# Kernel tuning notes

Measured on AMD Instinct MI355X. Metric: run time of the kernel, lower is better.

The kernel has to match this reference:

```python
import jax, jax.numpy as jnp
import numpy as np

# snntorch atan surrogate (alpha=2): forward heaviside, backward 1/(1+(pi*x)^2)
@jax.custom_vjp
def atan_spike(x):
    return (x > 0).astype(x.dtype)

def _atan_fwd(x):
    return atan_spike(x), x

def _atan_bwd(x, g):
    return (g / (1.0 + (jnp.pi * x) ** 2),)

atan_spike.defvjp(_atan_fwd, _atan_bwd)

B, S, D, H = 8, 2048, 1024, 1024

def setup_inputs() -> dict:
    key = jax.random.key(0)
    ks = jax.random.split(key, 6)
    s = 0.02
    return {
        "x": jax.random.normal(ks[0], (B, S, D), jnp.float32),
        "w_ih": jax.random.normal(ks[1], (4 * H, D), jnp.float32) * s,  # LSTMCell input weights (gate order i,f,g,o)
        "w_hh": jax.random.normal(ks[2], (4 * H, H), jnp.float32) * s,
        "b_ih": jnp.zeros((4 * H,), jnp.float32),
        "b_hh": jnp.zeros((4 * H,), jnp.float32),
        "w_fc": jax.random.normal(ks[3], (H, H), jnp.float32) * s,
        "b_fc": jnp.zeros((H,), jnp.float32),
        "threshold": jnp.float32(1.0),   # learn_threshold=True, init 1.0
        "dyt_alpha": jnp.float32(0.5),   # DynamicTanh alpha
        "dyt_w": jnp.ones((H,), jnp.float32),
        "dyt_b": jnp.zeros((H,), jnp.float32),
    }

def reference(x, w_ih, w_hh, b_ih, b_hh, w_fc, b_fc, threshold, dyt_alpha, dyt_w, dyt_b):
    # Precompute input-to-gate projection for all timesteps: (B,S,4H)
    x_ih = jnp.einsum("bsd,gd->bsg", x, w_ih) + b_ih

    def step(carry, inp):
        syn, mem = carry          # cell state, hidden/membrane state (B,H)
        x_t, g_ih = inp
        # subtract-reset based on PREVIOUS mem, detached (snntorch mem_reset)
        reset = jax.lax.stop_gradient((mem - threshold > 0).astype(mem.dtype))
        gates = g_ih + mem @ w_hh.T + b_hh
        i, f, g, o = jnp.split(gates, 4, axis=-1)
        c = jax.nn.sigmoid(f) * syn + jax.nn.sigmoid(i) * jnp.tanh(g)
        h = jax.nn.sigmoid(o) * jnp.tanh(c)
        mem_new = h - reset * threshold
        spk = atan_spike(mem_new - threshold)
        out = spk @ w_fc.T + b_fc + x_t                 # fc + residual
        out = dyt_w * jnp.tanh(dyt_alpha * out) + dyt_b  # Dyt normalizer
        return (c, mem_new), out

    syn0 = jnp.zeros((x.shape[0], w_fc.shape[0]), x.dtype)
    mem0 = jnp.zeros((x.shape[0], w_fc.shape[0]), x.dtype)
    (syn, mem), out = jax.lax.scan(
        step, (syn0, mem0),
        (jnp.swapaxes(x, 0, 1), jnp.swapaxes(x_ih, 0, 1)))
    return jnp.swapaxes(out, 0, 1), syn, mem
```

## Files before the change

kernel.cpp:

```cpp
#include <hip/hip_runtime.h>

#define NB 8
#define NS 2048
#define ND 1024
#define NH 1024
#define NWG 256
#define TPB 512
#define HPW 4
#define PSTRIDE 20

#define SCOPE_AGENT __HIP_MEMORY_SCOPE_AGENT

__device__ __forceinline__ float sigmf(float v)     { return 1.f / (1.f + __expf(-v)); }
__device__ __forceinline__ float tanh_fast(float v) { return 1.f - 2.f / (1.f + __expf(2.f * v)); }

#define DOT4(acc, W, V)                 \
    acc = fmaf((W).x, (V).x, acc);      \
    acc = fmaf((W).y, (V).y, acc);      \
    acc = fmaf((W).z, (V).z, acc);      \
    acc = fmaf((W).w, (V).w, acc);

__global__ __launch_bounds__(TPB, 2)
void scan_kernel(const float* __restrict__ x,
                 const float* __restrict__ w_ih,
                 const float* __restrict__ w_hh,
                 const float* __restrict__ b_ih,
                 const float* __restrict__ b_hh,
                 const float* __restrict__ thrp,
                 unsigned long long* __restrict__ membuf,
                 unsigned long long* __restrict__ bitmap,
                 float* __restrict__ out_syn,
                 float* __restrict__ out_mem)
{
    __shared__ float x_s2[2][NB * NH];
    __shared__ float m_s[NB * NH];
    __shared__ float sgm[16 * NB * PSTRIDE];
    __shared__ float sgx[2][16 * NB * PSTRIDE];
    __shared__ float bias_s[16];

    const int tid   = threadIdx.x;
    const int wg    = blockIdx.x;
    const int wave  = tid >> 6;
    const int lane  = tid & 63;
    const int g     = wave & 3;
    const bool ismem = (wave < 4);
    const float thr = *thrp;

    float4 wt[4][4];
    {
        const float* WM = ismem ? w_hh : w_ih;
        #pragma unroll
        for (int rl = 0; rl < 4; ++rl) {
            const int R = g * NH + wg * HPW + rl;
            #pragma unroll
            for (int j = 0; j < 4; ++j)
                wt[rl][j] = *(const float4*)(WM + (size_t)R * ND + j * 256 + lane * 4);
        }
    }
    if (tid < 16) {
        const int R = (tid >> 2) * NH + wg * HPW + (tid & 3);
        bias_s[tid] = b_ih[R] + b_hh[R];
    }
    float c_reg = 0.f;

    auto xdots = [&](int slot) {
        const float4* xs4 = (const float4*)x_s2[slot];
        #pragma unroll
        for (int b = 0; b < NB; ++b) {
            float4 xv[4];
            #pragma unroll
            for (int j = 0; j < 4; ++j) xv[j] = xs4[b * 256 + j * 64 + lane];
            float a0 = 0.f, a1 = 0.f, a2 = 0.f, a3 = 0.f;
            #pragma unroll
            for (int j = 0; j < 4; ++j) {
                DOT4(a0, wt[0][j], xv[j]);
                DOT4(a1, wt[1][j], xv[j]);
                DOT4(a2, wt[2][j], xv[j]);
                DOT4(a3, wt[3][j], xv[j]);
            }
            a0 += __shfl_xor(a0, 1); a0 += __shfl_xor(a0, 2);
            a1 += __shfl_xor(a1, 1); a1 += __shfl_xor(a1, 2);
            a2 += __shfl_xor(a2, 1); a2 += __shfl_xor(a2, 2);
            a3 += __shfl_xor(a3, 1); a3 += __shfl_xor(a3, 2);
            if ((lane & 3) == 0) {
                const int p = lane >> 2;
                float* dst = &sgx[slot][0];
                dst[((g * 4 + 0) * NB + b) * PSTRIDE + p] = a0;
                dst[((g * 4 + 1) * NB + b) * PSTRIDE + p] = a1;
                dst[((g * 4 + 2) * NB + b) * PSTRIDE + p] = a2;
                dst[((g * 4 + 3) * NB + b) * PSTRIDE + p] = a3;
            }
        }
    };

    auto prefetch = [&](int slot, int t1) {
        #pragma unroll
        for (int i = 0; i < 4; ++i) {
            const int q = i * 8 + wave;
            const int chunk = q * 64 + lane;
            const int b = chunk >> 8, d = (chunk & 255) * 4;
            __builtin_amdgcn_global_load_lds(
                (const __attribute__((address_space(1))) unsigned int*)(x + ((size_t)b * NS + t1) * ND + d),
                (__attribute__((address_space(3))) unsigned int*)&x_s2[slot][q * 256],
                16, 0, 0);
        }
    };

    prefetch(0, 0);
    __syncthreads();
    if (!ismem) xdots(0);

    for (int t = 0; t < NS; ++t) {
        const unsigned long long* mc = membuf + (size_t)(t & 1) * (NB * NH);
        unsigned long long*       mn64 = membuf + (size_t)((t + 1) & 1) * (NB * NH);

        if (t < NS - 1) prefetch((t + 1) & 1, t + 1);

        {
            const unsigned want = (unsigned)t;
            unsigned long long warr[16];
            #pragma unroll
            for (int k = 0; k < 16; ++k)
                warr[k] = __hip_atomic_load(mc + tid + k * TPB,
                                            __ATOMIC_RELAXED, SCOPE_AGENT);
            unsigned pend = 0;
            #pragma unroll
            for (int k = 0; k < 16; ++k) {
                if ((unsigned)(warr[k] >> 32) == want)
                    m_s[tid + k * TPB] = __uint_as_float((unsigned)warr[k]);
                else
                    pend |= (1u << k);
            }
            while (pend) {
                unsigned long long w2[16];
                unsigned np = 0;
                #pragma unroll
                for (int k = 0; k < 16; ++k)
                    if (pend & (1u << k))
                        w2[k] = __hip_atomic_load(mc + tid + k * TPB,
                                                  __ATOMIC_RELAXED, SCOPE_AGENT);
                #pragma unroll
                for (int k = 0; k < 16; ++k)
                    if (pend & (1u << k)) {
                        if ((unsigned)(w2[k] >> 32) == want)
                            m_s[tid + k * TPB] = __uint_as_float((unsigned)w2[k]);
                        else
                            np |= (1u << k);
                    }
                pend = np;
            }
        }
        __syncthreads();

        if (ismem) {
            const float4* ms4 = (const float4*)m_s;
            #pragma unroll
            for (int b = 0; b < NB; ++b) {
                float4 mv[4];
                #pragma unroll
                for (int j = 0; j < 4; ++j) mv[j] = ms4[b * 256 + j * 64 + lane];
                float a0 = 0.f, a1 = 0.f, a2 = 0.f, a3 = 0.f;
                #pragma unroll
                for (int j = 0; j < 4; ++j) {
                    DOT4(a0, wt[0][j], mv[j]);
                    DOT4(a1, wt[1][j], mv[j]);
                    DOT4(a2, wt[2][j], mv[j]);
                    DOT4(a3, wt[3][j], mv[j]);
                }
                a0 += __shfl_xor(a0, 1); a0 += __shfl_xor(a0, 2);
                a1 += __shfl_xor(a1, 1); a1 += __shfl_xor(a1, 2);
                a2 += __shfl_xor(a2, 1); a2 += __shfl_xor(a2, 2);
                a3 += __shfl_xor(a3, 1); a3 += __shfl_xor(a3, 2);
                if ((lane & 3) == 0) {
                    const int p = lane >> 2;
                    sgm[((g * 4 + 0) * NB + b) * PSTRIDE + p] = a0;
                    sgm[((g * 4 + 1) * NB + b) * PSTRIDE + p] = a1;
                    sgm[((g * 4 + 2) * NB + b) * PSTRIDE + p] = a2;
                    sgm[((g * 4 + 3) * NB + b) * PSTRIDE + p] = a3;
                }
            }
        } else if (t < NS - 1) {
            xdots((t + 1) & 1);
        }
        __syncthreads();

        if (tid < 32) {
            const int hl = tid >> 3, b = tid & 7;
            const int h  = wg * HPW + hl;
            float gv[4];
            #pragma unroll
            for (int gg = 0; gg < 4; ++gg) {
                const int r = gg * 4 + hl;
                const float4* pm = (const float4*)&sgm[(r * NB + b) * PSTRIDE];
                const float4* px = (const float4*)&sgx[t & 1][(r * NB + b) * PSTRIDE];
                float s = bias_s[r];
                #pragma unroll
                for (int q = 0; q < 4; ++q) {
                    float4 vm = pm[q], vx = px[q];
                    s += vm.x + vm.y + vm.z + vm.w + vx.x + vx.y + vx.z + vx.w;
                }
                gv[gg] = s;
            }
            const float cn = sigmf(gv[1]) * c_reg + sigmf(gv[0]) * tanh_fast(gv[2]);
            const float hv = sigmf(gv[3]) * tanh_fast(cn);
            const float mprev = m_s[b * NH + h];
            const float reset = (mprev - thr > 0.f) ? 1.f : 0.f;
            const float mn = hv - reset * thr;
            c_reg = cn;
            const unsigned long long pk =
                ((unsigned long long)(unsigned)(t + 1) << 32) | __float_as_uint(mn);
            __hip_atomic_store(mn64 + b * NH + h, pk, __ATOMIC_RELAXED, SCOPE_AGENT);
            if (mn - thr > 0.f)
                atomicOr(bitmap + (size_t)(b * NS + t) * (NH / 64) + (h >> 6),
                         1ull << (h & 63));
            if (t == NS - 1) {
                out_syn[b * NH + h] = cn;
                out_mem[b * NH + h] = mn;
            }
        }
        __syncthreads();
    }
}

__global__ __launch_bounds__(256)
void out_kernel(const float* __restrict__ x,
                const float* __restrict__ b_fc,
                const float* __restrict__ w_fc,
                const float* __restrict__ alphap,
                const float* __restrict__ dytw,
                const float* __restrict__ dytb,
                const unsigned long long* __restrict__ bitmap,
                float* __restrict__ out)
{
    __shared__ unsigned long long wds[16];
    __shared__ int flag;
    const int row = blockIdx.x;
    const int tid = threadIdx.x;
    if (tid < 16) wds[tid] = bitmap[(size_t)row * 16 + tid];
    __syncthreads();
    if (tid == 0) {
        unsigned long long o = 0ull;
        #pragma unroll
        for (int i = 0; i < 16; ++i) o |= wds[i];
        flag = (o != 0ull);
    }
    __syncthreads();

    const float alpha = *alphap;
    const float* xr = x + (size_t)row * NH;
    float* orow = out + (size_t)row * NH;
    const int j0 = tid * 4;

    float4 xv = *(const float4*)(xr + j0);
    float4 bf = *(const float4*)(b_fc + j0);
    float4 dw = *(const float4*)(dytw + j0);
    float4 db = *(const float4*)(dytb + j0);
    float p[4]   = {xv.x, xv.y, xv.z, xv.w};
    float bfa[4] = {bf.x, bf.y, bf.z, bf.w};
    float dwa[4] = {dw.x, dw.y, dw.z, dw.w};
    float dba[4] = {db.x, db.y, db.z, db.w};

    #pragma unroll
    for (int u = 0; u < 4; ++u) {
        float v = p[u] + bfa[u];
        if (flag) {
            const int j = j0 + u;
            for (int wi = 0; wi < 16; ++wi) {
                unsigned long long m = wds[wi];
                while (m) {
                    int bit = __ffsll(m) - 1;
                    m &= m - 1;
                    v += w_fc[(size_t)j * NH + wi * 64 + bit];
                }
            }
        }
        p[u] = dwa[u] * tanh_fast(alpha * v) + dba[u];
    }
    *(float4*)(orow + j0) = make_float4(p[0], p[1], p[2], p[3]);
}

extern "C" void kernel_launch(void* const* d_in, const int* in_sizes, int n_in,
                              void* d_out, int out_size, void* d_ws, size_t ws_size,
                              hipStream_t stream) {
    const float* x     = (const float*)d_in[0];
    const float* w_ih  = (const float*)d_in[1];
    const float* w_hh  = (const float*)d_in[2];
    const float* b_ih  = (const float*)d_in[3];
    const float* b_hh  = (const float*)d_in[4];
    const float* w_fc  = (const float*)d_in[5];
    const float* b_fc  = (const float*)d_in[6];
    const float* thr   = (const float*)d_in[7];
    const float* alpha = (const float*)d_in[8];
    const float* dytw  = (const float*)d_in[9];
    const float* dytb  = (const float*)d_in[10];

    float* out  = (float*)d_out;
    float* syn  = out + (size_t)NB * NS * NH;
    float* memf = syn + (size_t)NB * NH;

    char* ws = (char*)d_ws;
    unsigned long long* membuf = (unsigned long long*)ws;
    unsigned long long* bitmap = (unsigned long long*)(ws + 131072);

    size_t zbytes = 131072 + (size_t)NB * NS * (NH / 64) * 8;
    (void)hipMemsetAsync(d_ws, 0, zbytes, stream);

    hipLaunchKernelGGL(scan_kernel, dim3(NWG), dim3(TPB), 0, stream,
                       x, w_ih, w_hh, b_ih, b_hh, thr, membuf, bitmap, syn, memf);
    hipLaunchKernelGGL(out_kernel, dim3(NB * NS), dim3(256), 0, stream,
                       x, b_fc, w_fc, alpha, dytw, dytb, bitmap, out);
}
```

Baseline: 12.96 ms.

## Split batch across workgroup groups and pack recurrent state as tagged bf16

The 256 workgroups are split into two batch groups. Each workgroup now handles 4 batches and 8 hidden units with 1024 threads, instead of 8 batches and 4 hidden units. The exchanged membrane state shrinks from 64-bit (tag + fp32) to 32-bit (16-bit step tag + bf16 value). It is polled with one dwordx4 load per thread plus a sleep-backoff retry loop. This is meant to cut the per-step global read and sync traffic in the serial recurrence. The cost is reduced precision on the recurrent mem input to the w_hh matmul, which could flip spike decisions near threshold.

```diff
diff --git a/kernel.cpp b/kernel.cpp
--- a/kernel.cpp
+++ b/kernel.cpp
@@ -5,8 +5,9 @@
 #define ND 1024
 #define NH 1024
 #define NWG 256
-#define TPB 512
-#define HPW 4
+#define TPB 1024
+#define NBG 4
+#define HPW 8
 #define PSTRIDE 20
 
 #define SCOPE_AGENT __HIP_MEMORY_SCOPE_AGENT
@@ -20,30 +21,43 @@
     acc = fmaf((W).z, (V).z, acc);      \
     acc = fmaf((W).w, (V).w, acc);
 
-__global__ __launch_bounds__(TPB, 2)
+__device__ __forceinline__ float bf16_unpack(unsigned w) {
+    return __uint_as_float((w & 0xFFFFu) << 16);
+}
+__device__ __forceinline__ unsigned bf16_rne(float f) {
+    unsigned b = __float_as_uint(f);
+    return (b + 0x7FFFu + ((b >> 16) & 1u)) >> 16;
+}
+
+__global__ __launch_bounds__(TPB, 4)
 void scan_kernel(const float* __restrict__ x,
                  const float* __restrict__ w_ih,
                  const float* __restrict__ w_hh,
                  const float* __restrict__ b_ih,
                  const float* __restrict__ b_hh,
                  const float* __restrict__ thrp,
-                 unsigned long long* __restrict__ membuf,
+                 unsigned* __restrict__ membuf,
                  unsigned long long* __restrict__ bitmap,
                  float* __restrict__ out_syn,
                  float* __restrict__ out_mem)
 {
-    __shared__ float x_s2[2][NB * NH];
-    __shared__ float m_s[NB * NH];
-    __shared__ float sgm[16 * NB * PSTRIDE];
-    __shared__ float sgx[2][16 * NB * PSTRIDE];
-    __shared__ float bias_s[16];
+    __shared__ float x_s2[2][NBG * NH];
+    __shared__ float m_s[NBG * NH];
+    __shared__ float sgm[32 * NBG * PSTRIDE];
+    __shared__ float sgx[2][32 * NBG * PSTRIDE];
+    __shared__ float bias_s[32];
 
     const int tid   = threadIdx.x;
     const int wg    = blockIdx.x;
+    const int grpb  = wg >> 7;
+    const int wgl   = wg & 127;
+    const int hb    = wgl * HPW;
     const int wave  = tid >> 6;
     const int lane  = tid & 63;
-    const int g     = wave & 3;
-    const bool ismem = (wave < 4);
+    const bool ismem = (wave < 8);
+    const int wx    = wave & 7;
+    const int g     = wx & 3;
+    const int hh0   = (wx >> 2) * 4;
     const float thr = *thrp;
 
     float4 wt[4][4];
@@ -51,14 +65,14 @@
         const float* WM = ismem ? w_hh : w_ih;
         #pragma unroll
         for (int rl = 0; rl < 4; ++rl) {
-            const int R = g * NH + wg * HPW + rl;
+            const int R = g * NH + hb + hh0 + rl;
             #pragma unroll
             for (int j = 0; j < 4; ++j)
                 wt[rl][j] = *(const float4*)(WM + (size_t)R * ND + j * 256 + lane * 4);
         }
     }
-    if (tid < 16) {
-        const int R = (tid >> 2) * NH + wg * HPW + (tid & 3);
+    if (tid < 32) {
+        const int R = (tid >> 3) * NH + hb + (tid & 7);
         bias_s[tid] = b_ih[R] + b_hh[R];
     }
     float c_reg = 0.f;
@@ -66,10 +80,10 @@
     auto xdots = [&](int slot) {
         const float4* xs4 = (const float4*)x_s2[slot];
         #pragma unroll
-        for (int b = 0; b < NB; ++b) {
+        for (int bl = 0; bl < NBG; ++bl) {
             float4 xv[4];
             #pragma unroll
-            for (int j = 0; j < 4; ++j) xv[j] = xs4[b * 256 + j * 64 + lane];
+            for (int j = 0; j < 4; ++j) xv[j] = xs4[bl * 256 + j * 64 + lane];
             float a0 = 0.f, a1 = 0.f, a2 = 0.f, a3 = 0.f;
             #pragma unroll
             for (int j = 0; j < 4; ++j) {
@@ -85,25 +99,22 @@
             if ((lane & 3) == 0) {
                 const int p = lane >> 2;
                 float* dst = &sgx[slot][0];
-                dst[((g * 4 + 0) * NB + b) * PSTRIDE + p] = a0;
-                dst[((g * 4 + 1) * NB + b) * PSTRIDE + p] = a1;
-                dst[((g * 4 + 2) * NB + b) * PSTRIDE + p] = a2;
-                dst[((g * 4 + 3) * NB + b) * PSTRIDE + p] = a3;
+                const int r0 = g * 8 + hh0;
+                dst[((r0 + 0) * NBG + bl) * PSTRIDE + p] = a0;
+                dst[((r0 + 1) * NBG + bl) * PSTRIDE + p] = a1;
+                dst[((r0 + 2) * NBG + bl) * PSTRIDE + p] = a2;
+                dst[((r0 + 3) * NBG + bl) * PSTRIDE + p] = a3;
             }
         }
     };
 
     auto prefetch = [&](int slot, int t1) {
-        #pragma unroll
-        for (int i = 0; i < 4; ++i) {
-            const int q = i * 8 + wave;
-            const int chunk = q * 64 + lane;
-            const int b = chunk >> 8, d = (chunk & 255) * 4;
-            __builtin_amdgcn_global_load_lds(
-                (const __attribute__((address_space(1))) unsigned int*)(x + ((size_t)b * NS + t1) * ND + d),
-                (__attribute__((address_space(3))) unsigned int*)&x_s2[slot][q * 256],
-                16, 0, 0);
-        }
+        const int bl = tid >> 8, d = (tid & 255) * 4;
+        __builtin_amdgcn_global_load_lds(
+            (const __attribute__((address_space(1))) unsigned int*)
+                (x + ((size_t)(grpb * NBG + bl) * NS + t1) * ND + d),
+            (__attribute__((address_space(3))) unsigned int*)&x_s2[slot][tid * 4],
+            16, 0, 0);
     };
 
     prefetch(0, 0);
@@ -111,43 +122,28 @@
     if (!ismem) xdots(0);
 
     for (int t = 0; t < NS; ++t) {
-        const unsigned long long* mc = membuf + (size_t)(t & 1) * (NB * NH);
-        unsigned long long*       mn64 = membuf + (size_t)((t + 1) & 1) * (NB * NH);
-
-        if (t < NS - 1) prefetch((t + 1) & 1, t + 1);
+        const int cs = t & 1, ns_ = (t + 1) & 1;
+        const unsigned* mc = membuf + (size_t)(cs * 8 + grpb * NBG) * NH;
+        unsigned*       mp = membuf + (size_t)(ns_ * 8 + grpb * NBG) * NH;
+
+        if (t < NS - 1) prefetch(ns_, t + 1);
 
         {
             const unsigned want = (unsigned)t;
-            unsigned long long warr[16];
-            #pragma unroll
-            for (int k = 0; k < 16; ++k)
-                warr[k] = __hip_atomic_load(mc + tid + k * TPB,
-                                            __ATOMIC_RELAXED, SCOPE_AGENT);
-            unsigned pend = 0;
-            #pragma unroll
-            for (int k = 0; k < 16; ++k) {
-                if ((unsigned)(warr[k] >> 32) == want)
-                    m_s[tid + k * TPB] = __uint_as_float((unsigned)warr[k]);
-                else
-                    pend |= (1u << k);
-            }
-            while (pend) {
-                unsigned long long w2[16];
-                unsigned np = 0;
-                #pragma unroll
-                for (int k = 0; k < 16; ++k)
-                    if (pend & (1u << k))
-                        w2[k] = __hip_atomic_load(mc + tid + k * TPB,
-                                                  __ATOMIC_RELAXED, SCOPE_AGENT);
-                #pragma unroll
-                for (int k = 0; k < 16; ++k)
-                    if (pend & (1u << k)) {
-                        if ((unsigned)(w2[k] >> 32) == want)
-                            m_s[tid + k * TPB] = __uint_as_float((unsigned)w2[k]);
-                        else
-                            np |= (1u << k);
-                    }
-                pend = np;
+            uint4 v;
+            asm volatile(
+                "global_load_dwordx4 %0, %1, off sc0 sc1\n\t"
+                "s_waitcnt vmcnt(0)"
+                : "=&v"(v) : "v"(mc + tid * 4) : "memory");
+            unsigned w0 = v.x, w1 = v.y, w2 = v.z, w3 = v.w;
+            #pragma unroll
+            for (int k = 0; k < 4; ++k) {
+                unsigned w = (k == 0) ? w0 : (k == 1) ? w1 : (k == 2) ? w2 : w3;
+                while ((w >> 16) != want) {
+                    __builtin_amdgcn_s_sleep(1);
+                    w = __hip_atomic_load(mc + tid * 4 + k, __ATOMIC_RELAXED, SCOPE_AGENT);
+                }
+                m_s[tid * 4 + k] = bf16_unpack(w);
             }
         }
         __syncthreads();
@@ -155,10 +151,10 @@
         if (ismem) {
             const float4* ms4 = (const float4*)m_s;
             #pragma unroll
-            for (int b = 0; b < NB; ++b) {
+            for (int bl = 0; bl < NBG; ++bl) {
                 float4 mv[4];
                 #pragma unroll
-                for (int j = 0; j < 4; ++j) mv[j] = ms4[b * 256 + j * 64 + lane];
+                for (int j = 0; j < 4; ++j) mv[j] = ms4[bl * 256 + j * 64 + lane];
                 float a0 = 0.f, a1 = 0.f, a2 = 0.f, a3 = 0.f;
                 #pragma unroll
                 for (int j = 0; j < 4; ++j) {
@@ -173,26 +169,28 @@
                 a3 += __shfl_xor(a3, 1); a3 += __shfl_xor(a3, 2);
                 if ((lane & 3) == 0) {
                     const int p = lane >> 2;
-                    sgm[((g * 4 + 0) * NB + b) * PSTRIDE + p] = a0;
-                    sgm[((g * 4 + 1) * NB + b) * PSTRIDE + p] = a1;
-                    sgm[((g * 4 + 2) * NB + b) * PSTRIDE + p] = a2;
-                    sgm[((g * 4 + 3) * NB + b) * PSTRIDE + p] = a3;
+                    const int r0 = g * 8 + hh0;
+                    sgm[((r0 + 0) * NBG + bl) * PSTRIDE + p] = a0;
+                    sgm[((r0 + 1) * NBG + bl) * PSTRIDE + p] = a1;
+                    sgm[((r0 + 2) * NBG + bl) * PSTRIDE + p] = a2;
+                    sgm[((r0 + 3) * NBG + bl) * PSTRIDE + p] = a3;
                 }
             }
         } else if (t < NS - 1) {
-            xdots((t + 1) & 1);
+            xdots(ns_);
         }
         __syncthreads();
 
         if (tid < 32) {
-            const int hl = tid >> 3, b = tid & 7;
-            const int h  = wg * HPW + hl;
+            const int hl = tid >> 2, bl = tid & 3;
+            const int h  = hb + hl;
+            const int bg = grpb * NBG + bl;
             float gv[4];
             #pragma unroll
             for (int gg = 0; gg < 4; ++gg) {
-                const int r = gg * 4 + hl;
-                const float4* pm = (const float4*)&sgm[(r * NB + b) * PSTRIDE];
-                const float4* px = (const float4*)&sgx[t & 1][(r * NB + b) * PSTRIDE];
+                const int r = gg * 8 + hl;
+                const float4* pm = (const float4*)&sgm[(r * NBG + bl) * PSTRIDE];
+                const float4* px = (const float4*)&sgx[cs][(r * NBG + bl) * PSTRIDE];
                 float s = bias_s[r];
                 #pragma unroll
                 for (int q = 0; q < 4; ++q) {
@@ -203,19 +201,18 @@
             }
             const float cn = sigmf(gv[1]) * c_reg + sigmf(gv[0]) * tanh_fast(gv[2]);
             const float hv = sigmf(gv[3]) * tanh_fast(cn);
-            const float mprev = m_s[b * NH + h];
+            const float mprev = m_s[bl * NH + h];
             const float reset = (mprev - thr > 0.f) ? 1.f : 0.f;
             const float mn = hv - reset * thr;
             c_reg = cn;
-            const unsigned long long pk =
-                ((unsigned long long)(unsigned)(t + 1) << 32) | __float_as_uint(mn);
-            __hip_atomic_store(mn64 + b * NH + h, pk, __ATOMIC_RELAXED, SCOPE_AGENT);
+            const unsigned pk = ((unsigned)(t + 1) << 16) | bf16_rne(mn);
+            __hip_atomic_store(mp + bl * NH + h, pk, __ATOMIC_RELAXED, SCOPE_AGENT);
             if (mn - thr > 0.f)
-                atomicOr(bitmap + (size_t)(b * NS + t) * (NH / 64) + (h >> 6),
+                atomicOr(bitmap + (size_t)(bg * NS + t) * (NH / 64) + (h >> 6),
                          1ull << (h & 63));
             if (t == NS - 1) {
-                out_syn[b * NH + h] = cn;
-                out_mem[b * NH + h] = mn;
+                out_syn[bg * NH + h] = cn;
+                out_mem[bg * NH + h] = mn;
             }
         }
         __syncthreads();
@@ -299,10 +296,10 @@
     float* memf = syn + (size_t)NB * NH;
 
     char* ws = (char*)d_ws;
-    unsigned long long* membuf = (unsigned long long*)ws;
-    unsigned long long* bitmap = (unsigned long long*)(ws + 131072);
-
-    size_t zbytes = 131072 + (size_t)NB * NS * (NH / 64) * 8;
+    unsigned* membuf = (unsigned*)ws;
+    unsigned long long* bitmap = (unsigned long long*)(ws + 65536);
+
+    size_t zbytes = 65536 + (size_t)NB * NS * (NH / 64) * 8;
     (void)hipMemsetAsync(d_ws, 0, zbytes, stream);
 
     hipLaunchKernelGGL(scan_kernel, dim3(NWG), dim3(TPB), 0, stream,
```

Measured after the change: 11.26 ms. 1.15x faster.
